# Performance work log

Measured on AMD Instinct MI355X. Metric: run time of the kernel, lower is better.

The kernel has to match this reference:

```python
import jax, jax.numpy as jnp
import numpy as np

B, S1, S2, C = 8, 256, 256, 64
M1, M2 = 32, 32          # n_modes per spatial dim
SCALE = 1.0 / (C * C)    # 1/(in_channels*out_channels)


def setup_inputs() -> dict:
    key = jax.random.key(0)
    ks = jax.random.split(key, 5)
    X = jax.random.normal(ks[0], (B, S1, S2, C), dtype=jnp.float32)
    k0r = SCALE * jax.random.normal(ks[1], (M1, C, C), dtype=jnp.float32)
    k0i = SCALE * jax.random.normal(ks[2], (M1, C, C), dtype=jnp.float32)
    k1r = SCALE * jax.random.normal(ks[3], (M2, C, C), dtype=jnp.float32)
    k1i = SCALE * jax.random.normal(ks[4], (M2, C, C), dtype=jnp.float32)
    return {"X": X, "k0r": k0r, "k0i": k0i, "k1r": k1r, "k1i": k1i}


def reference(X, k0r, k0i, k1r, k1i):
    # Factorized spectral conv: per-spatial-dim rFFT -> truncated-mode
    # complex channel mix -> zero-pad -> irFFT, summed over dims.
    k0 = jax.lax.complex(k0r, k0i)  # (M1, out, in)
    k1 = jax.lax.complex(k1r, k1i)  # (M2, out, in)

    out = jnp.zeros_like(X)

    # --- spatial dim 0 (axis -3) ---
    Xf = jnp.fft.rfft(X, axis=-3, norm="forward")          # (B, S1//2+1, S2, C) complex
    Yt = jnp.einsum("rij,bryj->bryi", k0, Xf[:, :M1])       # truncated-mode channel mix
    Y = jnp.zeros_like(Xf).at[:, :M1].set(Yt)               # zero-pad back to full modes
    out = out + jnp.fft.irfft(Y, n=S1, axis=-3, norm="forward")

    # --- spatial dim 1 (axis -2) ---
    Xf = jnp.fft.rfft(X, axis=-2, norm="forward")           # (B, S1, S2//2+1, C)
    Yt = jnp.einsum("rij,bxrj->bxri", k1, Xf[:, :, :M2])
    Y = jnp.zeros_like(Xf).at[:, :, :M2].set(Yt)
    out = out + jnp.fft.irfft(Y, n=S2, axis=-2, norm="forward")

    return out
```

## Files before the change

kernel.cpp:

```cpp
#include <hip/hip_runtime.h>


namespace {

constexpr int S = 256, C = 64;

typedef _Float16 f16;
typedef _Float16 f16x2 __attribute__((ext_vector_type(2)));
typedef _Float16 f16x4 __attribute__((ext_vector_type(4)));
typedef _Float16 f16x8 __attribute__((ext_vector_type(8)));
typedef float f32x16 __attribute__((ext_vector_type(16)));

constexpr int OFF_FWDF = 0;
constexpr int OFF_INVF = 8192;
constexpr int OFF_A2   = 16384;
constexpr int OFF_PW   = 540672;
constexpr size_t WS_NEED = (size_t)OFF_PW * 4 + (size_t)8 * 256 * 256 * 64 * 2;

constexpr int P   = 4624;
constexpr int XFO = 8 * P;
constexpr int LDS_BYTES = 16 * P;

__device__ __host__ inline int cadr(int c) { return c * 16 + (c >> 3) * 16; }

__global__ void k_init_all(const float* __restrict__ k0r, const float* __restrict__ k0i,
                           const float* __restrict__ k1r, const float* __restrict__ ki1,
                           float* __restrict__ ws) {
  const int bid = blockIdx.x;
  if (bid < 128) {
    int t = bid * 256 + threadIdx.x;
    f16* fwdF = (f16*)(ws + OFF_FWDF);
    f16* invF = (f16*)(ws + OFF_INVF);
    if (t < 16384) {
      int e = t & 7, lane = (t >> 3) & 63, mtkk = t >> 9;
      int mt = mtkk & 1, kk = mtkk >> 1;
      int mc = mt * 32 + (lane & 31);
      int x = kk * 16 + 8 * (lane >> 5) + e;
      int r = mc >> 1;
      float ang = (float)((r * x) & 255) * (3.14159265358979323846f / 128.0f);
      float v = (mc & 1) ? -sinf(ang) : cosf(ang);
      fwdF[t] = (f16)v;
    } else {
      int t2 = t - 16384;
      int e = t2 & 7, lane = (t2 >> 3) & 63, mtg = (t2 >> 9) & 7, kk = t2 >> 12;
      int u = mtg * 32 + (lane & 31);
      int mcv = kk * 16 + 8 * (lane >> 5) + e;
      int r = mcv >> 1;
      float wgt = (r == 0) ? 1.0f : 2.0f;
      float ang = (float)((r * u) & 255) * (3.14159265358979323846f / 128.0f);
      float v = (mcv & 1) ? -wgt * sinf(ang) : wgt * cosf(ang);
      invF[t2] = (f16)(v * (1.0f / 256.0f));
    }
    return;
  }
  const int db = bid - 128;
  const float* kr = (db < 2048) ? k0r : k1r;
  const float* ki = (db < 2048) ? k0i : ki1;
  f16* A2 = (f16*)(ws + OFF_A2) + ((db < 2048) ? 0 : 524288);
  int t = (db & 2047) * 256 + threadIdx.x;
  int e = t & 7, l = (t >> 3) & 63, kk = (t >> 9) & 7, mt = (t >> 12) & 3, r = t >> 14;
  int m = mt * 32 + (l & 31);
  int kreal = kk * 16 + 8 * (l >> 5) + e;
  int i = m >> 1, imo = m & 1, j = kreal >> 1, imi = kreal & 1;
  int src = (r * 64 + i) * 64 + j;
  float v = (imi == 0) ? ((imo == 0) ? kr[src] : ki[src])
                       : ((imo == 0) ? -ki[src] : kr[src]);
  A2[t] = (f16)v;
}

template <int MODE>
__launch_bounds__(512, 2)
__global__ void k_dim(const float* __restrict__ X, const float* __restrict__ ws,
                      float* __restrict__ out, f16* __restrict__ pw) {
  constexpr int DIM = (MODE == 0 || MODE == 2) ? 0 : 1;
  __shared__ char sm[LDS_BYTES] __attribute__((aligned(16)));

  const int tid = threadIdx.x;
  const int l = tid & 63, w = tid >> 6;
  const int g2 = l >> 5, l31 = l & 31;
  const int n0 = w * 32;
  const int bid = (DIM == 1) ? (int)(gridDim.x - 1 - blockIdx.x) : (int)blockIdx.x;
  const int b = bid >> 6;
  const int t4 = (bid & 63) * 4;
  const size_t bbase = (size_t)b * (S * S * C);
  const f16* fwdF = (const f16*)(ws + OFF_FWDF);
  const f16* invF = (const f16*)(ws + OFF_INVF);
  const f16* A2 = (const f16*)(ws + OFF_A2) + (DIM == 0 ? 0 : 524288);

  auto gofs = [&](int u, int c) -> size_t {
    if (DIM == 0)
      return bbase + (size_t)u * (S * C) + (size_t)(t4 + (c >> 6)) * C + (c & 63);
    else
      return bbase + (size_t)(t4 + (c >> 6)) * (S * C) + (size_t)u * C + (c & 63);
  };

  const int ug = w >> 1;
  const int c1 = (w & 1) * 128 + l;
  const int c2 = c1 + 64;

  float r1[8], r2[8];
  auto stage_load = [&](int u0) {
#pragma unroll
    for (int j = 0; j < 8; ++j) r1[j] = X[gofs(u0 + ug * 8 + j, c1)];
#pragma unroll
    for (int j = 0; j < 8; ++j) r2[j] = X[gofs(u0 + ug * 8 + j, c2)];
  };
  auto stage_write = [&](int buf) {
    f16x8 v1, v2;
#pragma unroll
    for (int j = 0; j < 8; ++j) { v1[j] = (f16)r1[j]; v2[j] = (f16)r2[j]; }
    char* base = sm + buf * (4 * P) + ug * P;
    *(f16x8*)(base + cadr(c1)) = v1;
    *(f16x8*)(base + cadr(c2)) = v2;
  };

  f32x16 acc0, acc1;
#pragma unroll
  for (int q = 0; q < 16; ++q) { acc0[q] = 0.f; acc1[q] = 0.f; }

  stage_load(0);
  stage_write(0);
  __syncthreads();

  for (int ch = 0; ch < 8; ++ch) {
    if (ch < 7) stage_load((ch + 1) * 32);
    const char* bbuf = sm + (ch & 1) * (4 * P);
#pragma unroll
    for (int ks = 0; ks < 2; ++ks) {
      const int kk = ch * 2 + ks;
      f16x8 bf = *(const f16x8*)(bbuf + (ks * 2 + g2) * P + cadr(n0 + l31));
      f16x8 a0 = *(const f16x8*)(fwdF + ((size_t)(kk * 2 + 0) * 64 + l) * 8);
      f16x8 a1 = *(const f16x8*)(fwdF + ((size_t)(kk * 2 + 1) * 64 + l) * 8);
      acc0 = __builtin_amdgcn_mfma_f32_32x32x16_f16(a0, bf, acc0, 0, 0, 0);
      acc1 = __builtin_amdgcn_mfma_f32_32x32x16_f16(a1, bf, acc1, 0, 0, 0);
    }
    if (ch < 7) {
      stage_write((ch + 1) & 1);
      __syncthreads();
    }
  }
  __syncthreads();

  {
    const int col = n0 + l31;
    const int p = col >> 6, j = col & 63;
    const int kk = j >> 3, g2p = (j >> 2) & 1, js = j & 3;
#pragma unroll
    for (int pr = 0; pr < 16; ++pr) {
      const int q = (pr & 7) >> 1, hf = pr & 1;
      const int r = 2 * g2 + 4 * q + hf + (pr >> 3) * 16;
      const int reg = 4 * q + 2 * hf;
      const float v0 = (pr < 8) ? acc0[reg] : acc1[reg];
      const float v1 = (pr < 8) ? acc0[reg + 1] : acc1[reg + 1];
      f16x2 v2 = {(f16)v0, (f16)v1};
      const int W = (r * 16 + kk * 2 + g2p) * 4 + p;
      *(f16x2*)(sm + W * 16 + (W >> 3) * 16 + js * 4) = v2;
    }
  }
  __syncthreads();

  {
    const int colsel = l31 & 3;
#pragma unroll 1
    for (int rq = 0; rq < 4; ++rq) {
      const int r = w * 4 + rq;
      f16x8 bfr[8];
#pragma unroll
      for (int kk = 0; kk < 8; ++kk) {
        const int W = (r * 16 + kk * 2 + g2) * 4 + colsel;
        bfr[kk] = *(const f16x8*)(sm + W * 16 + (W >> 3) * 16);
      }
      char* yb = sm + XFO + w * P;
      const int ebyte = rq * 4;
#pragma unroll 1
      for (int mt = 0; mt < 4; ++mt) {
        f32x16 acc;
#pragma unroll
        for (int q = 0; q < 16; ++q) acc[q] = 0.f;
#pragma unroll
        for (int kk = 0; kk < 8; ++kk) {
          f16x8 af = *(const f16x8*)(A2 + ((size_t)((r * 4 + mt) * 8 + kk) * 64 + l) * 8);
          acc = __builtin_amdgcn_mfma_f32_32x32x16_f16(af, bfr[kk], acc, 0, 0, 0);
        }
        if (l31 < 4) {
#pragma unroll
          for (int t2 = 0; t2 < 8; ++t2) {
            int reg = t2 * 2;
            int rowin = (reg & 3) + 8 * (reg >> 2) + 4 * g2;
            int i = (mt * 32 + rowin) >> 1;
            f16x2 v2 = {(f16)acc[reg], (f16)acc[reg + 1]};
            *(f16x2*)(yb + cadr(l31 * 64 + i) + ebyte) = v2;
          }
        }
      }
    }
  }
  __syncthreads();

  const int colg = n0 + l31;
  const int pp = colg >> 6, jj = colg & 63;
  f16x8 bf4[4];
#pragma unroll
  for (int kk = 0; kk < 4; ++kk)
    bf4[kk] = *(const f16x8*)(sm + XFO + (kk * 2 + g2) * P + cadr(colg));

#pragma unroll 1
  for (int h = 0; h < 2; ++h) {
#pragma unroll 1
    for (int mt = 0; mt < 4; ++mt) {
      f32x16 a4;
#pragma unroll
      for (int q = 0; q < 16; ++q) a4[q] = 0.f;

#pragma unroll
      for (int kk = 0; kk < 4; ++kk) {
        f16x8 A = *(const f16x8*)(invF + ((size_t)(kk * 8 + h * 4 + mt) * 64 + l) * 8);
        a4 = __builtin_amdgcn_mfma_f32_32x32x16_f16(A, bf4[kk], a4, 0, 0, 0);
      }

      const int u0 = (h * 4 + mt) * 32;
#pragma unroll
      for (int reg = 0; reg < 16; ++reg) {
        const int u = u0 + (reg & 3) + 8 * (reg >> 2) + 4 * g2;
        size_t g = (DIM == 0)
                       ? bbase + (size_t)u * (S * C) + (size_t)(t4 + pp) * C + jj
                       : bbase + (size_t)(t4 + pp) * (S * C) + (size_t)u * C + jj;
        if (MODE == 0) out[g] = a4[reg];
        else if (MODE == 1) out[g] += a4[reg];
        else if (MODE == 2) pw[g] = (f16)a4[reg];
        else out[g] = a4[reg] + (float)pw[g];
      }
    }
  }
}

}

extern "C" void kernel_launch(void* const* d_in, const int* in_sizes, int n_in,
                              void* d_out, int out_size, void* d_ws, size_t ws_size,
                              hipStream_t stream) {
  (void)in_sizes; (void)n_in; (void)out_size;
  const float* X   = (const float*)d_in[0];
  const float* k0r = (const float*)d_in[1];
  const float* k0i = (const float*)d_in[2];
  const float* k1r = (const float*)d_in[3];
  const float* k1i = (const float*)d_in[4];
  float* out = (float*)d_out;
  float* ws  = (float*)d_ws;
  f16* pw = (f16*)(ws + OFF_PW);

  k_init_all<<<4224, 256, 0, stream>>>(k0r, k0i, k1r, k1i, ws);
  if (ws_size >= WS_NEED) {
    k_dim<2><<<512, 512, 0, stream>>>(X, ws, out, pw);
    k_dim<3><<<512, 512, 0, stream>>>(X, ws, out, pw);
  } else {
    k_dim<0><<<512, 512, 0, stream>>>(X, ws, out, nullptr);
    k_dim<1><<<512, 512, 0, stream>>>(X, ws, out, nullptr);
  }
}
```

Baseline: 149.5 us.

## Re-layout f16 partial buffer for vectorized prefetch in second-dim pass

Changes the layout of the f16 intermediate written by the dim-0 pass so that the dim-1 pass can read four contiguous values per lane as f16x4. Those reads are issued early, before the channel-mix and inverse MFMA stages, to hide their latency. The final loops are also fully unrolled and launch bounds are raised to 4 blocks per CU. The prefetch arrays add many registers, which conflicts with the tighter launch bound and risks spills.

```diff
diff --git a/kernel.cpp b/kernel.cpp
--- a/kernel.cpp
+++ b/kernel.cpp
@@ -69,7 +69,7 @@
 }
 
 template <int MODE>
-__launch_bounds__(512, 2)
+__launch_bounds__(512, 4)
 __global__ void k_dim(const float* __restrict__ X, const float* __restrict__ ws,
                       float* __restrict__ out, f16* __restrict__ pw) {
   constexpr int DIM = (MODE == 0 || MODE == 2) ? 0 : 1;
@@ -87,6 +87,10 @@
   const f16* invF = (const f16*)(ws + OFF_INVF);
   const f16* A2 = (const f16*)(ws + OFF_A2) + (DIM == 0 ? 0 : 524288);
 
+  const int colg = n0 + l31;
+  const int pp = colg >> 6, jj = colg & 63;
+  f16x4 pfA[4][4], pfB[4][4];
+
   auto gofs = [&](int u, int c) -> size_t {
     if (DIM == 0)
       return bbase + (size_t)u * (S * C) + (size_t)(t4 + (c >> 6)) * C + (c & 63);
@@ -159,6 +163,15 @@
   }
   __syncthreads();
 
+  if constexpr (MODE == 3) {
+    const f16* pwb = pw + bbase + (size_t)(t4 + pp) * 256 + (size_t)jj * 4;
+#pragma unroll
+    for (int mt = 0; mt < 4; ++mt)
+#pragma unroll
+      for (int q = 0; q < 4; ++q)
+        pfA[mt][q] = *(const f16x4*)(pwb + (size_t)(mt * 8 + 2 * q + g2) * 65536);
+  }
+
   {
     const int colsel = l31 & 3;
 #pragma unroll 1
@@ -197,16 +210,23 @@
   }
   __syncthreads();
 
-  const int colg = n0 + l31;
-  const int pp = colg >> 6, jj = colg & 63;
+  if constexpr (MODE == 3) {
+    const f16* pwb = pw + bbase + (size_t)(t4 + pp) * 256 + (size_t)jj * 4;
+#pragma unroll
+    for (int mt = 0; mt < 4; ++mt)
+#pragma unroll
+      for (int q = 0; q < 4; ++q)
+        pfB[mt][q] = *(const f16x4*)(pwb + (size_t)(32 + mt * 8 + 2 * q + g2) * 65536);
+  }
+
   f16x8 bf4[4];
 #pragma unroll
   for (int kk = 0; kk < 4; ++kk)
     bf4[kk] = *(const f16x8*)(sm + XFO + (kk * 2 + g2) * P + cadr(colg));
 
-#pragma unroll 1
+#pragma unroll
   for (int h = 0; h < 2; ++h) {
-#pragma unroll 1
+#pragma unroll
     for (int mt = 0; mt < 4; ++mt) {
       f32x16 a4;
 #pragma unroll
@@ -222,13 +242,21 @@
 #pragma unroll
       for (int reg = 0; reg < 16; ++reg) {
         const int u = u0 + (reg & 3) + 8 * (reg >> 2) + 4 * g2;
-        size_t g = (DIM == 0)
-                       ? bbase + (size_t)u * (S * C) + (size_t)(t4 + pp) * C + jj
-                       : bbase + (size_t)(t4 + pp) * (S * C) + (size_t)u * C + jj;
-        if (MODE == 0) out[g] = a4[reg];
-        else if (MODE == 1) out[g] += a4[reg];
-        else if (MODE == 2) pw[g] = (f16)a4[reg];
-        else out[g] = a4[reg] + (float)pw[g];
+        if constexpr (MODE == 2) {
+          size_t pwi = bbase + (size_t)(t4 >> 2) * 65536 + (size_t)u * 256 +
+                       (size_t)jj * 4 + pp;
+          pw[pwi] = (f16)a4[reg];
+        } else if constexpr (MODE == 3) {
+          size_t g = bbase + (size_t)(t4 + pp) * (S * C) + (size_t)u * C + jj;
+          const f16x4& pv = (h == 0) ? pfA[mt][reg >> 2] : pfB[mt][reg >> 2];
+          out[g] = a4[reg] + (float)pv[reg & 3];
+        } else {
+          size_t g = (DIM == 0)
+                         ? bbase + (size_t)u * (S * C) + (size_t)(t4 + pp) * C + jj
+                         : bbase + (size_t)(t4 + pp) * (S * C) + (size_t)u * C + jj;
+          if constexpr (MODE == 0) out[g] = a4[reg];
+          else                     out[g] += a4[reg];
+        }
       }
     }
   }
```

Result: slower. 183.2 us (+22.6%).
